# Kernel optimization log

Measured on AMD Instinct MI355X. Metric: run time of the kernel, lower is better.

The kernel has to match this reference:

```python
import jax, jax.numpy as jnp
import numpy as np

N, E, C, RB, H = 10000, 160000, 64, 8, 64
AVG_NEIGH = 16.0


def _sph(v):
    # component-normalized real spherical harmonics l=1,2,3 of unit vectors v [E,3]
    x, y, z = v[..., 0], v[..., 1], v[..., 2]
    s3, s5, s15 = 3.0 ** 0.5, 5.0 ** 0.5, 15.0 ** 0.5
    y1 = s3 * jnp.stack([x, y, z], -1)  # [E,3]
    y2 = jnp.stack([
        s15 * x * y,
        s15 * y * z,
        0.5 * s5 * (3.0 * z * z - 1.0),
        s15 * x * z,
        0.5 * s15 * (x * x - y * y),
    ], -1)  # [E,5]
    c1 = (35.0 / 8.0) ** 0.5
    c2 = 105.0 ** 0.5
    c3 = (21.0 / 8.0) ** 0.5
    c4 = (7.0 ** 0.5) / 2.0
    y3 = jnp.stack([
        c1 * y * (3.0 * x * x - y * y),
        c2 * x * y * z,
        c3 * y * (5.0 * z * z - 1.0),
        c4 * z * (5.0 * z * z - 3.0),
        c3 * x * (5.0 * z * z - 1.0),
        0.5 * c2 * z * (x * x - y * y),
        c1 * x * (x * x - y * y),
    ], -1)  # [E,7]
    return y1, y2, y3


def setup_inputs() -> dict:
    key = jax.random.key(0)
    ks = jax.random.split(key, 12)
    inp = {
        'vectors': jax.random.normal(ks[0], (E, 3), jnp.float32),
        'node_feats': jax.random.normal(ks[1], (N, C), jnp.float32),
        'radial_embedding': jax.random.normal(ks[2], (E, RB), jnp.float32),
        'W_up': jax.random.normal(ks[3], (C, C), jnp.float32) / np.sqrt(C),
        'mlp_w1': jax.random.normal(ks[4], (RB, H), jnp.float32) / np.sqrt(RB),
        'mlp_w2': jax.random.normal(ks[5], (H, H), jnp.float32) / np.sqrt(H),
        'mlp_w3': jax.random.normal(ks[6], (H, H), jnp.float32) / np.sqrt(H),
        'mlp_w4': jax.random.normal(ks[7], (H, 4 * C), jnp.float32) / np.sqrt(H),
        'W_down': jax.random.normal(ks[8], (4, C, C), jnp.float32) / np.sqrt(C),
        'senders': jax.random.randint(ks[9], (E,), 0, N, jnp.int32),
        'receivers': jax.random.randint(ks[10], (E,), 0, N, jnp.int32),
    }
    return inp


def reference(vectors, node_feats, radial_embedding, W_up, mlp_w1, mlp_w2, mlp_w3, mlp_w4, W_down, senders, receivers):
    n = node_feats.shape[0]
    # linear_up (scalars: plain channel mixing)
    x = node_feats @ W_up                                   # [N,C]
    sf = x[senders]                                         # [E,C] gather
    u = vectors / (jnp.linalg.norm(vectors, axis=-1, keepdims=True) + 1e-12)
    y1, y2, y3 = _sph(u)
    # radial MLP -> per-irrep mixing weights [E, 4C]
    h = jax.nn.silu(radial_embedding @ mlp_w1)
    h = jax.nn.silu(h @ mlp_w2)
    h = jax.nn.silu(h @ mlp_w3)
    mix = h @ mlp_w4
    m0, m1, m2, m3 = jnp.split(mix, 4, axis=-1)             # each [E,C]
    # tensor product of Cx0e with Y_l -> Cx(l), scaled by radial mix
    msg0 = sf * m0                                          # [E,C]
    msg1 = (sf * m1)[:, :, None] * y1[:, None, :]           # [E,C,3]
    msg2 = (sf * m2)[:, :, None] * y2[:, None, :]           # [E,C,5]
    msg3 = (sf * m3)[:, :, None] * y3[:, None, :]           # [E,C,7]
    inv = 1.0 / jnp.sqrt(jnp.asarray(AVG_NEIGH, msg0.dtype))
    seg = lambda m: jax.ops.segment_sum(m, receivers, num_segments=n) * inv
    o0, o1, o2, o3 = seg(msg0), seg(msg1), seg(msg2), seg(msg3)
    # linear_down: per-l channel mixing
    o0 = o0 @ W_down[0]
    o1 = jnp.einsum('ncm,cd->ndm', o1, W_down[1])
    o2 = jnp.einsum('ncm,cd->ndm', o2, W_down[2])
    o3 = jnp.einsum('ncm,cd->ndm', o3, W_down[3])
    return jnp.concatenate([o0, o1.reshape(n, -1), o2.reshape(n, -1), o3.reshape(n, -1)], axis=-1)  # [N, 16C]
```

## Files before the change

### kernel.cpp

```cpp
#include <hip/hip_runtime.h>
#include <math.h>

#define CC 64
typedef _Float16 f16;
typedef _Float16 half8_t __attribute__((ext_vector_type(8)));
typedef float f32x4 __attribute__((ext_vector_type(4)));

__device__ __forceinline__ float silu_f(float v) {
    return v / (1.0f + __expf(-v));
}

__global__ void k_up(const float* __restrict__ nf, const float* __restrict__ Wup,
                     float* __restrict__ x, int N) {
    int tid = blockIdx.x * blockDim.x + threadIdx.x;
    if (tid >= N * CC) return;
    int n = tid >> 6;
    int j = tid & 63;
    const float* nfr = nf + (size_t)n * CC;
    float acc = 0.f;
#pragma unroll
    for (int k = 0; k < CC; ++k) acc += nfr[k] * Wup[k * CC + j];
    x[tid] = acc;
}

__global__ __launch_bounds__(256) void k_mlp(const float* __restrict__ rad,
        const float* __restrict__ w1, const float* __restrict__ w2,
        const float* __restrict__ w3, const float* __restrict__ w4,
        f16* __restrict__ mixb, int E) {
    __shared__ f16 wB[64][72];
    __shared__ f16 wC[64][72];
    __shared__ f16 act[128][72];

    int t = threadIdx.x;
    int e0 = blockIdx.x * 128;
    int lane = t & 63;
    int wid = t >> 6;

    {
        int n = t & 63;
        int k0 = t >> 6;
        for (int k = k0; k < 64; k += 4) {
            wB[n][k] = (f16)w2[k * 64 + n];
            wC[n][k] = (f16)w3[k * 64 + n];
        }
    }

    {
        int i = t & 127;
        int jh = (t >> 7) * 32;
        int e = e0 + i;
        float r[8];
        if (e < E) {
#pragma unroll
            for (int k = 0; k < 8; ++k) r[k] = rad[(size_t)e * 8 + k];
        } else {
#pragma unroll
            for (int k = 0; k < 8; ++k) r[k] = 0.f;
        }
        float a[32];
#pragma unroll
        for (int j = 0; j < 32; ++j) a[j] = 0.f;
#pragma unroll
        for (int k = 0; k < 8; ++k) {
            float rv = r[k];
#pragma unroll
            for (int j = 0; j < 32; ++j) a[j] += rv * w1[k * 64 + jh + j];
        }
#pragma unroll
        for (int jj = 0; jj < 32; jj += 8) {
            half8_t h;
#pragma unroll
            for (int u = 0; u < 8; ++u) h[u] = (f16)silu_f(a[jj + u]);
            *(half8_t*)&act[i][jh + jj] = h;
        }
    }
    __syncthreads();

    int m0 = wid * 32;
    int fm = lane & 15;
    int q  = lane >> 4;

    auto loadA = [&](int mbase, int kc) -> half8_t {
        return *(const half8_t*)&act[mbase + fm][kc + q * 8];
    };

    {
        half8_t a00 = loadA(m0, 0),      a01 = loadA(m0, 32);
        half8_t a10 = loadA(m0 + 16, 0), a11 = loadA(m0 + 16, 32);
#pragma unroll
        for (int nt = 0; nt < 4; ++nt) {
            half8_t b0 = *(const half8_t*)&wB[nt * 16 + fm][q * 8];
            half8_t b1 = *(const half8_t*)&wB[nt * 16 + fm][32 + q * 8];
            f32x4 c0 = {0.f, 0.f, 0.f, 0.f};
            c0 = __builtin_amdgcn_mfma_f32_16x16x32_f16(a00, b0, c0, 0, 0, 0);
            c0 = __builtin_amdgcn_mfma_f32_16x16x32_f16(a01, b1, c0, 0, 0, 0);
            f32x4 c1 = {0.f, 0.f, 0.f, 0.f};
            c1 = __builtin_amdgcn_mfma_f32_16x16x32_f16(a10, b0, c1, 0, 0, 0);
            c1 = __builtin_amdgcn_mfma_f32_16x16x32_f16(a11, b1, c1, 0, 0, 0);
#pragma unroll
            for (int r = 0; r < 4; ++r) {
                act[m0 + q * 4 + r][nt * 16 + fm]      = (f16)silu_f(c0[r]);
                act[m0 + 16 + q * 4 + r][nt * 16 + fm] = (f16)silu_f(c1[r]);
            }
        }
    }

    {
        half8_t a00 = loadA(m0, 0),      a01 = loadA(m0, 32);
        half8_t a10 = loadA(m0 + 16, 0), a11 = loadA(m0 + 16, 32);
#pragma unroll
        for (int nt = 0; nt < 4; ++nt) {
            half8_t b0 = *(const half8_t*)&wC[nt * 16 + fm][q * 8];
            half8_t b1 = *(const half8_t*)&wC[nt * 16 + fm][32 + q * 8];
            f32x4 c0 = {0.f, 0.f, 0.f, 0.f};
            c0 = __builtin_amdgcn_mfma_f32_16x16x32_f16(a00, b0, c0, 0, 0, 0);
            c0 = __builtin_amdgcn_mfma_f32_16x16x32_f16(a01, b1, c0, 0, 0, 0);
            f32x4 c1 = {0.f, 0.f, 0.f, 0.f};
            c1 = __builtin_amdgcn_mfma_f32_16x16x32_f16(a10, b0, c1, 0, 0, 0);
            c1 = __builtin_amdgcn_mfma_f32_16x16x32_f16(a11, b1, c1, 0, 0, 0);
#pragma unroll
            for (int r = 0; r < 4; ++r) {
                act[m0 + q * 4 + r][nt * 16 + fm]      = (f16)silu_f(c0[r]);
                act[m0 + 16 + q * 4 + r][nt * 16 + fm] = (f16)silu_f(c1[r]);
            }
        }
    }

    half8_t A00 = loadA(m0, 0),      A01 = loadA(m0, 32);
    half8_t A10 = loadA(m0 + 16, 0), A11 = loadA(m0 + 16, 32);

    auto do_l = [&](int l, f16 (*w)[72]) {
#pragma unroll
        for (int nt = 0; nt < 4; ++nt) {
            half8_t b0 = *(const half8_t*)&w[nt * 16 + fm][q * 8];
            half8_t b1 = *(const half8_t*)&w[nt * 16 + fm][32 + q * 8];
            f32x4 c0 = {0.f, 0.f, 0.f, 0.f};
            c0 = __builtin_amdgcn_mfma_f32_16x16x32_f16(A00, b0, c0, 0, 0, 0);
            c0 = __builtin_amdgcn_mfma_f32_16x16x32_f16(A01, b1, c0, 0, 0, 0);
            f32x4 c1 = {0.f, 0.f, 0.f, 0.f};
            c1 = __builtin_amdgcn_mfma_f32_16x16x32_f16(A10, b0, c1, 0, 0, 0);
            c1 = __builtin_amdgcn_mfma_f32_16x16x32_f16(A11, b1, c1, 0, 0, 0);
            int col = l * 64 + nt * 16 + fm;
#pragma unroll
            for (int r = 0; r < 4; ++r) {
                int er0 = e0 + m0 + q * 4 + r;
                int er1 = er0 + 16;
                if (er0 < E) mixb[(size_t)er0 * 256 + col] = (f16)c0[r];
                if (er1 < E) mixb[(size_t)er1 * 256 + col] = (f16)c1[r];
            }
        }
    };

    __syncthreads();
    {
        int n = t & 63;
        int k0 = t >> 6;
        for (int k = k0; k < 64; k += 4) {
            wB[n][k] = (f16)w4[k * 256 + n];
            wC[n][k] = (f16)w4[k * 256 + 64 + n];
        }
    }
    __syncthreads();
    do_l(0, wB);
    do_l(1, wC);
    __syncthreads();
    {
        int n = t & 63;
        int k0 = t >> 6;
        for (int k = k0; k < 64; k += 4) {
            wB[n][k] = (f16)w4[k * 256 + 128 + n];
            wC[n][k] = (f16)w4[k * 256 + 192 + n];
        }
    }
    __syncthreads();
    do_l(2, wB);
    do_l(3, wC);
}

__global__ void k_hist(const int* __restrict__ rcv, int* __restrict__ cnt, int E) {
    int e = blockIdx.x * blockDim.x + threadIdx.x;
    if (e < E) atomicAdd(&cnt[rcv[e]], 1);
}

__global__ __launch_bounds__(1024) void k_scan(const int* __restrict__ cnt,
        int* __restrict__ off, int* __restrict__ cur, int N) {
    __shared__ int buf[1024];
    __shared__ int s_carry;
    int t = threadIdx.x;
    if (t == 0) s_carry = 0;
    __syncthreads();
    for (int base = 0; base < N; base += 1024) {
        int i = base + t;
        int v = (i < N) ? cnt[i] : 0;
        buf[t] = v;
        __syncthreads();
        for (int d = 1; d < 1024; d <<= 1) {
            int add = (t >= d) ? buf[t - d] : 0;
            __syncthreads();
            buf[t] += add;
            __syncthreads();
        }
        int excl = buf[t] - v + s_carry;
        if (i < N) { off[i] = excl; cur[i] = excl; }
        __syncthreads();
        if (t == 1023) s_carry += buf[1023];
        __syncthreads();
    }
    if (t == 0) off[N] = s_carry;
}

__global__ void k_fill(const int* __restrict__ rcv, int* __restrict__ cur,
                       int* __restrict__ eid, int E) {
    int e = blockIdx.x * blockDim.x + threadIdx.x;
    if (e < E) {
        int p = atomicAdd(&cur[rcv[e]], 1);
        eid[p] = e;
    }
}

__global__ __launch_bounds__(256) void k_gather(const float* __restrict__ x,
        const f16* __restrict__ mixb, const float* __restrict__ vec,
        const int* __restrict__ snd, const int* __restrict__ eid,
        const int* __restrict__ off, const float* __restrict__ Wd,
        float* __restrict__ out, int N) {
    __shared__ float sbuf[4][1024];
    int wv = threadIdx.x >> 6;
    int lane = threadIdx.x & 63;
    int n = blockIdx.x * 4 + wv;
    if (n >= N) return;

    const float s3 = 1.7320508075688772f;
    const float s5 = 2.2360679774997896f;
    const float s15 = 3.8729833462074170f;
    const float c1 = 2.0916500663351889f;
    const float c2 = 10.246950765959598f;
    const float c3 = 1.6201851746019651f;
    const float c4 = 1.3228756555322954f;

    float o[16];
#pragma unroll
    for (int i = 0; i < 16; ++i) o[i] = 0.f;

    int beg = off[n], end = off[n + 1];
    for (int i = beg; i < end; ++i) {
        int e = eid[i];
        int s = snd[e];
        float vx = vec[(size_t)e * 3 + 0];
        float vy = vec[(size_t)e * 3 + 1];
        float vz = vec[(size_t)e * 3 + 2];
        float nrm = sqrtf(vx * vx + vy * vy + vz * vz) + 1e-12f;
        float rinv = 1.0f / nrm;
        float ux = vx * rinv, uy = vy * rinv, uz = vz * rinv;

        float zz = uz * uz, xx = ux * ux, yy = uy * uy;
        float y10 = s3 * ux, y11 = s3 * uy, y12 = s3 * uz;
        float y20 = s15 * ux * uy;
        float y21 = s15 * uy * uz;
        float y22 = 0.5f * s5 * (3.f * zz - 1.f);
        float y23 = s15 * ux * uz;
        float y24 = 0.5f * s15 * (xx - yy);
        float y30 = c1 * uy * (3.f * xx - yy);
        float y31 = c2 * ux * uy * uz;
        float y32 = c3 * uy * (5.f * zz - 1.f);
        float y33 = c4 * uz * (5.f * zz - 3.f);
        float y34 = c3 * ux * (5.f * zz - 1.f);
        float y35 = 0.5f * c2 * uz * (xx - yy);
        float y36 = c1 * ux * (xx - yy);

        float sf = x[(size_t)s * 64 + lane];
        const f16* mr = mixb + (size_t)e * 256;
        float t0 = sf * (float)mr[lane];
        float t1 = sf * (float)mr[64 + lane];
        float t2 = sf * (float)mr[128 + lane];
        float t3 = sf * (float)mr[192 + lane];

        o[0]  += t0;
        o[1]  += t1 * y10;
        o[2]  += t1 * y11;
        o[3]  += t1 * y12;
        o[4]  += t2 * y20;
        o[5]  += t2 * y21;
        o[6]  += t2 * y22;
        o[7]  += t2 * y23;
        o[8]  += t2 * y24;
        o[9]  += t3 * y30;
        o[10] += t3 * y31;
        o[11] += t3 * y32;
        o[12] += t3 * y33;
        o[13] += t3 * y34;
        o[14] += t3 * y35;
        o[15] += t3 * y36;
    }

#pragma unroll
    for (int t = 0; t < 16; ++t) sbuf[wv][t * 64 + lane] = o[t];

    float d[16];
#pragma unroll
    for (int i = 0; i < 16; ++i) d[i] = 0.f;
#pragma unroll 1
    for (int c = 0; c < 64; ++c) {
        float w0 = Wd[c * 64 + lane];
        float w1r = Wd[4096 + c * 64 + lane];
        float w2r = Wd[8192 + c * 64 + lane];
        float w3r = Wd[12288 + c * 64 + lane];
        const float* sb = &sbuf[wv][c];
        d[0] += sb[0] * w0;
#pragma unroll
        for (int m = 0; m < 3; ++m) d[1 + m] += sb[(1 + m) * 64] * w1r;
#pragma unroll
        for (int m = 0; m < 5; ++m) d[4 + m] += sb[(4 + m) * 64] * w2r;
#pragma unroll
        for (int m = 0; m < 7; ++m) d[9 + m] += sb[(9 + m) * 64] * w3r;
    }

    float* outr = out + (size_t)n * 1024;
    outr[lane] = 0.25f * d[0];
#pragma unroll
    for (int m = 0; m < 3; ++m) outr[64 + lane * 3 + m] = 0.25f * d[1 + m];
#pragma unroll
    for (int m = 0; m < 5; ++m) outr[256 + lane * 5 + m] = 0.25f * d[4 + m];
#pragma unroll
    for (int m = 0; m < 7; ++m) outr[576 + lane * 7 + m] = 0.25f * d[9 + m];
}

extern "C" void kernel_launch(void* const* d_in, const int* in_sizes, int n_in,
                              void* d_out, int out_size, void* d_ws, size_t ws_size,
                              hipStream_t stream) {
    const float* vectors    = (const float*)d_in[0];
    const float* node_feats = (const float*)d_in[1];
    const float* radial     = (const float*)d_in[2];
    const float* W_up       = (const float*)d_in[3];
    const float* w1         = (const float*)d_in[4];
    const float* w2         = (const float*)d_in[5];
    const float* w3         = (const float*)d_in[6];
    const float* w4         = (const float*)d_in[7];
    const float* Wd         = (const float*)d_in[8];
    const int*   snd        = (const int*)d_in[9];
    const int*   rcv        = (const int*)d_in[10];
    float* out = (float*)d_out;

    int E = in_sizes[9];
    int N = in_sizes[1] / CC;

    float* ws   = (float*)d_ws;
    float* x    = ws;
    f16*   mixb = (f16*)(x + (size_t)N * 64);
    int*   cnt  = (int*)((char*)mixb + (size_t)E * 256 * sizeof(f16));
    int*   off  = cnt + N;
    int*   cur  = off + (N + 1);
    int*   eid  = cur + N;

    hipMemsetAsync(cnt, 0, (size_t)N * sizeof(int), stream);

    k_up<<<(N * CC + 255) / 256, 256, 0, stream>>>(node_feats, W_up, x, N);
    k_hist<<<(E + 255) / 256, 256, 0, stream>>>(rcv, cnt, E);
    k_scan<<<1, 1024, 0, stream>>>(cnt, off, cur, N);
    k_fill<<<(E + 255) / 256, 256, 0, stream>>>(rcv, cur, eid, E);
    k_mlp<<<(E + 127) / 128, 256, 0, stream>>>(radial, w1, w2, w3, w4, mixb, E);
    k_gather<<<(N + 3) / 4, 256, 0, stream>>>(x, mixb, vectors, snd, eid, off, Wd, out, N);
}
```

Before: 267.2 us.

## Write MLP mix and spherical harmonics in receiver-sorted order for streaming gather

```diff
diff --git a/kernel.cpp b/kernel.cpp
--- a/kernel.cpp
+++ b/kernel.cpp
@@ -23,10 +23,102 @@
     x[tid] = acc;
 }
 
+__global__ void k_hist(const int* __restrict__ rcv, int* __restrict__ cnt, int E) {
+    int e = blockIdx.x * blockDim.x + threadIdx.x;
+    if (e < E) atomicAdd(&cnt[rcv[e]], 1);
+}
+
+__global__ __launch_bounds__(1024) void k_scan(const int* __restrict__ cnt,
+        int* __restrict__ off, int* __restrict__ cur, int N) {
+    __shared__ int wsum[16];
+    __shared__ int carry;
+    int t = threadIdx.x;
+    int wave = t >> 6, lane = t & 63;
+    if (t == 0) carry = 0;
+    __syncthreads();
+    for (int base = 0; base < N; base += 1024) {
+        int i = base + t;
+        int v = (i < N) ? cnt[i] : 0;
+        int sc = v;
+#pragma unroll
+        for (int d = 1; d < 64; d <<= 1) {
+            int u = __shfl_up(sc, d, 64);
+            if (lane >= d) sc += u;
+        }
+        if (lane == 63) wsum[wave] = sc;
+        __syncthreads();
+        if (wave == 0) {
+            int w = (lane < 16) ? wsum[lane] : 0;
+            int s2 = w;
+#pragma unroll
+            for (int d = 1; d < 16; d <<= 1) {
+                int u = __shfl_up(s2, d, 64);
+                if (lane >= d) s2 += u;
+            }
+            if (lane < 16) wsum[lane] = s2;
+        }
+        __syncthreads();
+        int wexcl = (wave == 0) ? 0 : wsum[wave - 1];
+        int excl = carry + wexcl + (sc - v);
+        if (i < N) { off[i] = excl; cur[i] = excl; }
+        __syncthreads();
+        if (t == 0) carry += wsum[15];
+        __syncthreads();
+    }
+    if (t == 0) off[N] = carry;
+}
+
+__global__ void k_fill(const int* __restrict__ rcv, const int* __restrict__ snd,
+                       int* __restrict__ cur, int* __restrict__ eid,
+                       int* __restrict__ pos, int* __restrict__ sndp, int E) {
+    int e = blockIdx.x * blockDim.x + threadIdx.x;
+    if (e < E) {
+        int p = atomicAdd(&cur[rcv[e]], 1);
+        eid[p] = e;
+        pos[e] = p;
+        sndp[p] = snd[e];
+    }
+}
+
+__global__ void k_sph(const int* __restrict__ eid, const float* __restrict__ vec,
+                      float* __restrict__ yb, int E) {
+    int i = blockIdx.x * blockDim.x + threadIdx.x;
+    if (i >= E) return;
+    int e = eid[i];
+    float vx = vec[(size_t)e * 3 + 0];
+    float vy = vec[(size_t)e * 3 + 1];
+    float vz = vec[(size_t)e * 3 + 2];
+    float nrm = sqrtf(vx * vx + vy * vy + vz * vz) + 1e-12f;
+    float rinv = 1.0f / nrm;
+    float ux = vx * rinv, uy = vy * rinv, uz = vz * rinv;
+
+    const float s3 = 1.7320508075688772f;
+    const float s5 = 2.2360679774997896f;
+    const float s15 = 3.8729833462074170f;
+    const float c1 = 2.0916500663351889f;
+    const float c2 = 10.246950765959598f;
+    const float c3 = 1.6201851746019651f;
+    const float c4 = 1.3228756555322954f;
+
+    float zz = uz * uz, xx = ux * ux, yy = uy * uy;
+    float4 r0 = {1.0f, s3 * ux, s3 * uy, s3 * uz};
+    float4 r1 = {s15 * ux * uy, s15 * uy * uz, 0.5f * s5 * (3.f * zz - 1.f),
+                 s15 * ux * uz};
+    float4 r2 = {0.5f * s15 * (xx - yy), c1 * uy * (3.f * xx - yy),
+                 c2 * ux * uy * uz, c3 * uy * (5.f * zz - 1.f)};
+    float4 r3 = {c4 * uz * (5.f * zz - 3.f), c3 * ux * (5.f * zz - 1.f),
+                 0.5f * c2 * uz * (xx - yy), c1 * ux * (xx - yy)};
+    float* yr = yb + (size_t)i * 16;
+    *(float4*)(yr + 0)  = r0;
+    *(float4*)(yr + 4)  = r1;
+    *(float4*)(yr + 8)  = r2;
+    *(float4*)(yr + 12) = r3;
+}
+
 __global__ __launch_bounds__(256) void k_mlp(const float* __restrict__ rad,
         const float* __restrict__ w1, const float* __restrict__ w2,
         const float* __restrict__ w3, const float* __restrict__ w4,
-        f16* __restrict__ mixb, int E) {
+        const int* __restrict__ pos, f16* __restrict__ mixp, int E) {
     __shared__ f16 wB[64][72];
     __shared__ f16 wC[64][72];
     __shared__ f16 act[128][72];
@@ -140,13 +232,20 @@
             f32x4 c1 = {0.f, 0.f, 0.f, 0.f};
             c1 = __builtin_amdgcn_mfma_f32_16x16x32_f16(A10, b0, c1, 0, 0, 0);
             c1 = __builtin_amdgcn_mfma_f32_16x16x32_f16(A11, b1, c1, 0, 0, 0);
-            int col = l * 64 + nt * 16 + fm;
 #pragma unroll
             for (int r = 0; r < 4; ++r) {
-                int er0 = e0 + m0 + q * 4 + r;
-                int er1 = er0 + 16;
-                if (er0 < E) mixb[(size_t)er0 * 256 + col] = (f16)c0[r];
-                if (er1 < E) mixb[(size_t)er1 * 256 + col] = (f16)c1[r];
+                act[m0 + q * 4 + r][nt * 16 + fm]      = (f16)c0[r];
+                act[m0 + 16 + q * 4 + r][nt * 16 + fm] = (f16)c1[r];
+            }
+        }
+#pragma unroll
+        for (int it = 0; it < 4; ++it) {
+            int row = (lane >> 3) + it * 8;
+            int er = e0 + m0 + row;
+            if (er < E) {
+                int p = pos[er];
+                half8_t v = *(const half8_t*)&act[m0 + row][(lane & 7) * 8];
+                *(half8_t*)&mixp[(size_t)p * 256 + l * 64 + (lane & 7) * 8] = v;
             }
         }
     };
@@ -177,127 +276,62 @@
     do_l(3, wC);
 }
 
-__global__ void k_hist(const int* __restrict__ rcv, int* __restrict__ cnt, int E) {
-    int e = blockIdx.x * blockDim.x + threadIdx.x;
-    if (e < E) atomicAdd(&cnt[rcv[e]], 1);
-}
-
-__global__ __launch_bounds__(1024) void k_scan(const int* __restrict__ cnt,
-        int* __restrict__ off, int* __restrict__ cur, int N) {
-    __shared__ int buf[1024];
-    __shared__ int s_carry;
-    int t = threadIdx.x;
-    if (t == 0) s_carry = 0;
-    __syncthreads();
-    for (int base = 0; base < N; base += 1024) {
-        int i = base + t;
-        int v = (i < N) ? cnt[i] : 0;
-        buf[t] = v;
-        __syncthreads();
-        for (int d = 1; d < 1024; d <<= 1) {
-            int add = (t >= d) ? buf[t - d] : 0;
-            __syncthreads();
-            buf[t] += add;
-            __syncthreads();
-        }
-        int excl = buf[t] - v + s_carry;
-        if (i < N) { off[i] = excl; cur[i] = excl; }
-        __syncthreads();
-        if (t == 1023) s_carry += buf[1023];
-        __syncthreads();
-    }
-    if (t == 0) off[N] = s_carry;
-}
-
-__global__ void k_fill(const int* __restrict__ rcv, int* __restrict__ cur,
-                       int* __restrict__ eid, int E) {
-    int e = blockIdx.x * blockDim.x + threadIdx.x;
-    if (e < E) {
-        int p = atomicAdd(&cur[rcv[e]], 1);
-        eid[p] = e;
-    }
-}
-
 __global__ __launch_bounds__(256) void k_gather(const float* __restrict__ x,
-        const f16* __restrict__ mixb, const float* __restrict__ vec,
-        const int* __restrict__ snd, const int* __restrict__ eid,
-        const int* __restrict__ off, const float* __restrict__ Wd,
-        float* __restrict__ out, int N) {
+        const f16* __restrict__ mixp, const float* __restrict__ yb,
+        const int* __restrict__ sndp, const int* __restrict__ off,
+        const float* __restrict__ Wd, float* __restrict__ out, int N) {
     __shared__ float sbuf[4][1024];
     int wv = threadIdx.x >> 6;
     int lane = threadIdx.x & 63;
     int n = blockIdx.x * 4 + wv;
     if (n >= N) return;
 
-    const float s3 = 1.7320508075688772f;
-    const float s5 = 2.2360679774997896f;
-    const float s15 = 3.8729833462074170f;
-    const float c1 = 2.0916500663351889f;
-    const float c2 = 10.246950765959598f;
-    const float c3 = 1.6201851746019651f;
-    const float c4 = 1.3228756555322954f;
-
     float o[16];
 #pragma unroll
     for (int i = 0; i < 16; ++i) o[i] = 0.f;
 
-    int beg = off[n], end = off[n + 1];
-    for (int i = beg; i < end; ++i) {
-        int e = eid[i];
-        int s = snd[e];
-        float vx = vec[(size_t)e * 3 + 0];
-        float vy = vec[(size_t)e * 3 + 1];
-        float vz = vec[(size_t)e * 3 + 2];
-        float nrm = sqrtf(vx * vx + vy * vy + vz * vz) + 1e-12f;
-        float rinv = 1.0f / nrm;
-        float ux = vx * rinv, uy = vy * rinv, uz = vz * rinv;
-
-        float zz = uz * uz, xx = ux * ux, yy = uy * uy;
-        float y10 = s3 * ux, y11 = s3 * uy, y12 = s3 * uz;
-        float y20 = s15 * ux * uy;
-        float y21 = s15 * uy * uz;
-        float y22 = 0.5f * s5 * (3.f * zz - 1.f);
-        float y23 = s15 * ux * uz;
-        float y24 = 0.5f * s15 * (xx - yy);
-        float y30 = c1 * uy * (3.f * xx - yy);
-        float y31 = c2 * ux * uy * uz;
-        float y32 = c3 * uy * (5.f * zz - 1.f);
-        float y33 = c4 * uz * (5.f * zz - 3.f);
-        float y34 = c3 * ux * (5.f * zz - 1.f);
-        float y35 = 0.5f * c2 * uz * (xx - yy);
-        float y36 = c1 * ux * (xx - yy);
-
+    auto process = [&](int i) {
+        int s = sndp[i];
+        const float* yr = yb + (size_t)i * 16;
+        float4 A = *(const float4*)(yr + 0);
+        float4 B = *(const float4*)(yr + 4);
+        float4 Cv = *(const float4*)(yr + 8);
+        float4 D = *(const float4*)(yr + 12);
         float sf = x[(size_t)s * 64 + lane];
-        const f16* mr = mixb + (size_t)e * 256;
+        const f16* mr = mixp + (size_t)i * 256;
         float t0 = sf * (float)mr[lane];
         float t1 = sf * (float)mr[64 + lane];
         float t2 = sf * (float)mr[128 + lane];
         float t3 = sf * (float)mr[192 + lane];
-
         o[0]  += t0;
-        o[1]  += t1 * y10;
-        o[2]  += t1 * y11;
-        o[3]  += t1 * y12;
-        o[4]  += t2 * y20;
-        o[5]  += t2 * y21;
-        o[6]  += t2 * y22;
-        o[7]  += t2 * y23;
-        o[8]  += t2 * y24;
-        o[9]  += t3 * y30;
-        o[10] += t3 * y31;
-        o[11] += t3 * y32;
-        o[12] += t3 * y33;
-        o[13] += t3 * y34;
-        o[14] += t3 * y35;
-        o[15] += t3 * y36;
-    }
+        o[1]  += t1 * A.y;
+        o[2]  += t1 * A.z;
+        o[3]  += t1 * A.w;
+        o[4]  += t2 * B.x;
+        o[5]  += t2 * B.y;
+        o[6]  += t2 * B.z;
+        o[7]  += t2 * B.w;
+        o[8]  += t2 * Cv.x;
+        o[9]  += t3 * Cv.y;
+        o[10] += t3 * Cv.z;
+        o[11] += t3 * Cv.w;
+        o[12] += t3 * D.x;
+        o[13] += t3 * D.y;
+        o[14] += t3 * D.z;
+        o[15] += t3 * D.w;
+    };
+
+    int beg = off[n], end = off[n + 1];
+    int i = beg;
+    for (; i + 1 < end; i += 2) { process(i); process(i + 1); }
+    if (i < end) process(i);
 
 #pragma unroll
     for (int t = 0; t < 16; ++t) sbuf[wv][t * 64 + lane] = o[t];
 
     float d[16];
 #pragma unroll
-    for (int i = 0; i < 16; ++i) d[i] = 0.f;
+    for (int i2 = 0; i2 < 16; ++i2) d[i2] = 0.f;
 #pragma unroll 1
     for (int c = 0; c < 64; ++c) {
         float w0 = Wd[c * 64 + lane];
@@ -345,18 +379,22 @@
 
     float* ws   = (float*)d_ws;
     float* x    = ws;
-    f16*   mixb = (f16*)(x + (size_t)N * 64);
-    int*   cnt  = (int*)((char*)mixb + (size_t)E * 256 * sizeof(f16));
+    float* yb   = x + (size_t)N * 64;
+    f16*   mixp = (f16*)(yb + (size_t)E * 16);
+    int*   cnt  = (int*)((char*)mixp + (size_t)E * 256 * sizeof(f16));
     int*   off  = cnt + N;
     int*   cur  = off + (N + 1);
     int*   eid  = cur + N;
+    int*   pos  = eid + E;
+    int*   sndp = pos + E;
 
     hipMemsetAsync(cnt, 0, (size_t)N * sizeof(int), stream);
 
     k_up<<<(N * CC + 255) / 256, 256, 0, stream>>>(node_feats, W_up, x, N);
     k_hist<<<(E + 255) / 256, 256, 0, stream>>>(rcv, cnt, E);
     k_scan<<<1, 1024, 0, stream>>>(cnt, off, cur, N);
-    k_fill<<<(E + 255) / 256, 256, 0, stream>>>(rcv, cur, eid, E);
-    k_mlp<<<(E + 127) / 128, 256, 0, stream>>>(radial, w1, w2, w3, w4, mixb, E);
-    k_gather<<<(N + 3) / 4, 256, 0, stream>>>(x, mixb, vectors, snd, eid, off, Wd, out, N);
-}
+    k_fill<<<(E + 255) / 256, 256, 0, stream>>>(rcv, snd, cur, eid, pos, sndp, E);
+    k_sph<<<(E + 255) / 256, 256, 0, stream>>>(eid, vectors, yb, E);
+    k_mlp<<<(E + 127) / 128, 256, 0, stream>>>(radial, w1, w2, w3, w4, pos, mixp, E);
+    k_gather<<<(N + 3) / 4, 256, 0, stream>>>(x, mixp, yb, sndp, off, Wd, out, N);
+}
```

Result: faster. 253.7 us (-5.1%).
